# Kernel tuning notes

Measured on AMD Instinct MI355X. Metric: run time of the kernel, lower is better.

The kernel has to match this reference:

```python
import jax, jax.numpy as jnp
import numpy as np

B, H, W, N = 8, 384, 384, 96
STEPSZ = 0.1; ALPHA = 0.01; BETA = 0.01; STD = 1.0
NSTEPS = 50; NSTEPS_W = 10; DMAX = 15.0; EXTGRADFAC = 10.0

def make_gauss_edge_fltr(std):
    # Gaussian-derivative edge filters, one per spatial dim: [2,1,k,k]
    r = int(np.ceil(3 * std)); t = np.arange(-r, r + 1, dtype=np.float32)
    g = np.exp(-t * t / (2 * std * std)); g /= g.sum()
    dg = -t / (std * std) * np.exp(-t * t / (2 * std * std)); dg /= np.abs(dg).sum()
    fy = np.outer(dg, g)   # d/drow
    fx = np.outer(g, dg)   # d/dcol
    return np.stack([fy, fx])[:, None].astype(np.float32)

def setup_inputs() -> dict:
    key = jax.random.key(0)
    k1, k2 = jax.random.split(key, 2)
    pred_dmap = jax.random.normal(k1, (B, 1, H, W), jnp.float32)
    nodes = jax.random.uniform(k2, (B, N, 2), jnp.float32)
    nodes = nodes * jnp.array([H - 1.0, W - 1.0], jnp.float32)
    nodes = jnp.sort(nodes, axis=1)  # roughly monotone chain -> path-like snake
    widths = jnp.ones((B, N), jnp.float32) * 3.0
    fltr = jnp.asarray(make_gauss_edge_fltr(STD))
    return {"pred_dmap": pred_dmap, "nodes": nodes, "widths": widths, "fltr": fltr}

def grad_im(x, fltr):
    # x: [B,1,H,W], fltr: [2,1,k,k] -> [B,2,H,W]
    return jax.lax.conv_general_dilated(x, fltr, (1, 1), 'SAME',
                                        dimension_numbers=('NCHW', 'OIHW', 'NCHW'))

def interp(img, pts):
    # bilinear sample: img [C,H,W], pts [N,2] (row,col) -> [N,C]
    C, Hh, Ww = img.shape
    y = jnp.clip(pts[:, 0], 0.0, Hh - 1.0); x = jnp.clip(pts[:, 1], 0.0, Ww - 1.0)
    y0 = jnp.floor(y).astype(jnp.int32); x0 = jnp.floor(x).astype(jnp.int32)
    y1 = jnp.minimum(y0 + 1, Hh - 1); x1 = jnp.minimum(x0 + 1, Ww - 1)
    wy = y - y0; wx = x - x0
    v00 = img[:, y0, x0]; v01 = img[:, y0, x1]
    v10 = img[:, y1, x0]; v11 = img[:, y1, x1]
    v = v00 * (1 - wy) * (1 - wx) + v01 * (1 - wy) * wx + v10 * wy * (1 - wx) + v11 * wy * wx
    return v.T

def d2_open(x):
    # second difference with replicated endpoints (open snake)
    xp = jnp.concatenate([x[:1], x, x[-1:]], 0)
    return xp[:-2] - 2 * xp[1:-1] + xp[2:]

def snake_one(nodes, widths, g, gw):
    # explicit active-contour iterations on node positions
    def pstep(x, _):
        fext = interp(g, x)                       # [N,2] external force
        d2 = d2_open(x); d4 = d2_open(d2)
        return x + STEPSZ * (ALPHA * d2 - BETA * d4 + fext), None
    x, _ = jax.lax.scan(pstep, nodes, None, length=NSTEPS)
    # unit normals from central-difference tangents
    t = jnp.concatenate([x[1:2] - x[0:1], 0.5 * (x[2:] - x[:-2]), x[-1:] - x[-2:-1]], 0)
    n = jnp.stack([-t[:, 1], t[:, 0]], 1)
    n = n / (jnp.linalg.norm(n, axis=1, keepdims=True) + 1e-6)
    def wstep(w, _):
        gp = interp(gw, x + w[:, None] * n); gm = interp(gw, x - w[:, None] * n)
        f = 0.5 * (jnp.sum(gp * n, 1) - jnp.sum(gm * n, 1))
        return jnp.maximum(w + STEPSZ * f, 0.5), None
    w, _ = jax.lax.scan(wstep, widths, None, length=NSTEPS_W)
    return x, w

def render(x, w):
    # distance-to-ribbon map, clipped at DMAX; only [HW,S] intermediates
    ys, xs = jnp.meshgrid(jnp.arange(H, dtype=jnp.float32),
                          jnp.arange(W, dtype=jnp.float32), indexing='ij')
    P = jnp.stack([ys.ravel(), xs.ravel()], 1)          # [HW,2]
    a = x[:-1]; ab = x[1:] - a                          # [S,2]
    denom = jnp.sum(ab * ab, 1) + 1e-8                  # [S]
    dotpa = P @ ab.T - jnp.sum(a * ab, 1)               # [HW,S] = (P-a).ab
    t = jnp.clip(dotpa / denom, 0.0, 1.0)
    pa2 = jnp.sum(P * P, 1)[:, None] - 2 * (P @ a.T) + jnp.sum(a * a, 1)  # |P-a|^2
    d = jnp.sqrt(jnp.maximum(pa2 - 2 * t * dotpa + t * t * denom, 0.0))
    ws = 0.5 * (w[:-1] + w[1:])                         # per-segment width
    dmap = jnp.min(jnp.maximum(d - ws, 0.0), axis=1)
    return jnp.minimum(dmap, DMAX).reshape(H, W)

def reference(pred_dmap, nodes, widths, fltr):
    gimg = grad_im(pred_dmap, fltr) * EXTGRADFAC          # [B,2,H,W]
    gimgW = grad_im(jnp.abs(pred_dmap), fltr) * EXTGRADFAC
    def per_sample(nd, wd, g, gw):
        x, w = snake_one(nd, wd, g, gw)
        return render(x, w)
    dm = jax.vmap(per_sample)(nodes, widths, gimg, gimgW)[:, None]  # [B,1,H,W]
    dm = jax.lax.stop_gradient(dm)   # snake_dm.detach() in the original
    return jnp.mean((pred_dmap - dm) ** 2)
```

## Files before the change

### kernel.cpp

```cpp
#include <hip/hip_runtime.h>
#include <math.h>

#define BB   8
#define HH   384
#define WW   384
#define NN   96
#define HWSZ (HH * WW)
#define NSEG (NN - 1)
#define SEGF 12
#define SEGPAD 1152
#define DMAXV 15.0f
#define ROWS_PER_BLK 12
#define NCHUNK (HH / ROWS_PER_BLK)
#define CROWS 12
#define CBANDS (HH / CROWS)
#define MAGICU 0x9E3779B9u

typedef unsigned long long u64;
typedef unsigned int u32;

__device__ inline void st_pair(float* p, float lo, float hi)
{
    u64 v = ((u64)__float_as_uint(hi) << 32) | (u64)__float_as_uint(lo);
    __hip_atomic_store((u64*)p, v, __ATOMIC_RELAXED, __HIP_MEMORY_SCOPE_AGENT);
}

__device__ inline float ld_f32_coh(const float* p)
{
    u32 v = __hip_atomic_load((u32*)p, __ATOMIC_RELAXED, __HIP_MEMORY_SCOPE_AGENT);
    return __uint_as_float(v);
}

#define WAIT_ALL() asm volatile("s_waitcnt vmcnt(0) lgkmcnt(0)" ::: "memory")

__device__ inline void load_taps(const float* __restrict__ fltr,
                                 float* __restrict__ sg, float* __restrict__ sdg)
{
    int tid = threadIdx.x;
    if (tid < 7) {
        float s = 0.f;
#pragma unroll
        for (int i = 0; i < 7; ++i) s += fabsf(fltr[i * 7 + tid]);
        sg[tid] = s;
    } else if (tid < 14) {
        int r = tid - 7;
        float s = 0.f;
#pragma unroll
        for (int j = 0; j < 7; ++j) s += fltr[r * 7 + j];
        sdg[r] = s;
    }
    __syncthreads();
}

__device__ inline float2 bilin2i(const float2* __restrict__ img, float py, float px)
{
    float y = fminf(fmaxf(py, 0.0f), (float)(HH - 1));
    float x = fminf(fmaxf(px, 0.0f), (float)(WW - 1));
    int y0 = (int)floorf(y);
    int x0 = (int)floorf(x);
    int y1 = min(y0 + 1, HH - 1);
    bool xedge = (x0 + 1 > WW - 1);
    float wy = y - (float)y0;
    float wx = x - (float)x0;
    float4 r0 = *(const float4*)(img + y0 * WW + x0);
    float4 r1 = *(const float4*)(img + y1 * WW + x0);
    float2 v00 = make_float2(r0.x, r0.y);
    float2 v01 = xedge ? v00 : make_float2(r0.z, r0.w);
    float2 v10 = make_float2(r1.x, r1.y);
    float2 v11 = xedge ? v10 : make_float2(r1.z, r1.w);
    float w00 = (1.f - wy) * (1.f - wx);
    float w01 = (1.f - wy) * wx;
    float w10 = wy * (1.f - wx);
    float w11 = wy * wx;
    return make_float2(v00.x * w00 + v01.x * w01 + v10.x * w10 + v11.x * w11,
                       v00.y * w00 + v01.y * w01 + v10.y * w10 + v11.y * w11);
}

__device__ inline void write_seg_wt(float* __restrict__ r,
                                    float py, float px, float qy, float qx, float wseg)
{
    float aby = qy - py, abx = qx - px;
    float denom = aby * aby + abx * abx + 1e-8f;
    float aab = py * aby + px * abx;
    float aa  = py * py + px * px;
    float reach = DMAXV + wseg;
    st_pair(r + 0,  py,  px);
    st_pair(r + 2,  aby, abx);
    st_pair(r + 4,  aab, denom);
    st_pair(r + 6,  1.0f / denom, aa);
    st_pair(r + 8,  wseg, fminf(py, qy) - reach);
    st_pair(r + 10, fmaxf(py, qy) + reach, 0.f);
}

__global__ __launch_bounds__(384) void snake_fused(
    const float* __restrict__ pred, const float* __restrict__ nodes,
    const float* __restrict__ widths, const float* __restrict__ fltr,
    float* __restrict__ g2f, float* __restrict__ gw2f,
    float* __restrict__ segs, u64* __restrict__ pflag,
    u32* __restrict__ convflag, u32* __restrict__ segflag,
    float* __restrict__ out)
{
    __shared__ float sg[7], sdg[7];
    __shared__ float ss[NSEG * SEGF];
    __shared__ int slo, shi;
    __shared__ float swsum[6];

    int blk = blockIdx.x;
    int b   = blk & 7;
    int band = blk >> 3;
    int t = threadIdx.x;

    load_taps(fltr, sg, sdg);

    {
        int y0 = band * CROWS;
        int x = t;
        const float* pb = pred + (size_t)b * HWSZ;
        bool xin = (x >= 3) && (x < WW - 3);

        float hg[7], hd[7], hga[7], hda[7];

#pragma unroll
        for (int q = 0; q < CROWS + 6; ++q) {
            float vg = 0.f, vd = 0.f, vga = 0.f, vda = 0.f;
            int r = y0 + q - 3;
            if (r >= 0 && r < HH) {
                const float* row = pb + r * WW;
                if (xin) {
#pragma unroll
                    for (int k = 0; k < 7; ++k) {
                        float v  = row[x + k - 3];
                        float av = fabsf(v);
                        vg  = fmaf(v,  sg[k],  vg);
                        vd  = fmaf(v,  sdg[k], vd);
                        vga = fmaf(av, sg[k],  vga);
                        vda = fmaf(av, sdg[k], vda);
                    }
                } else {
#pragma unroll
                    for (int k = 0; k < 7; ++k) {
                        int ix = x + k - 3;
                        float v  = (ix >= 0 && ix < WW) ? row[ix] : 0.f;
                        float av = fabsf(v);
                        vg  = fmaf(v,  sg[k],  vg);
                        vd  = fmaf(v,  sdg[k], vd);
                        vga = fmaf(av, sg[k],  vga);
                        vda = fmaf(av, sdg[k], vda);
                    }
                }
            }
            hg[q % 7] = vg; hd[q % 7] = vd; hga[q % 7] = vga; hda[q % 7] = vda;

            if (q >= 6) {
                int y = y0 + q - 6;
                float o0 = 0.f, o1 = 0.f, o2 = 0.f, o3 = 0.f;
#pragma unroll
                for (int j = 0; j < 7; ++j) {
                    int s = (q - 6 + j) % 7;
                    o0 = fmaf(hg[s],  sdg[j], o0);
                    o1 = fmaf(hd[s],  sg[j],  o1);
                    o2 = fmaf(hga[s], sdg[j], o2);
                    o3 = fmaf(hda[s], sg[j],  o3);
                }
                size_t gi = (size_t)b * HWSZ + (size_t)y * WW + x;
                st_pair(g2f  + 2 * gi, o0 * 10.f, o1 * 10.f);
                st_pair(gw2f + 2 * gi, o2 * 10.f, o3 * 10.f);
            }
        }
    }
    WAIT_ALL();
    __syncthreads();
    if (t == 0)
        __hip_atomic_store(&convflag[blk], MAGICU,
                           __ATOMIC_RELAXED, __HIP_MEMORY_SCOPE_AGENT);

    if (blk < 8 && t < 64) {
        while (__hip_atomic_load(&convflag[b + 8 * (t & 31)],
                                 __ATOMIC_RELAXED, __HIP_MEMORY_SCOPE_AGENT) != MAGICU)
            __builtin_amdgcn_s_sleep(2);
        asm volatile("" ::: "memory");

        const float2* gb  = (const float2*)g2f  + (size_t)b * HWSZ;
        const float2* gwb = (const float2*)gw2f + (size_t)b * HWSZ;
        const int HALF = NN / 2;
        bool act = (t < HALF);
        bool t0 = (t == 0), tl = (t == HALF - 1);

        float ay = 0.f, ax = 0.f, by = 0.f, bx = 0.f;
        if (act) {
            float4 n4 = *(const float4*)(nodes + (size_t)(b * NN + 2 * t) * 2);
            ay = n4.x; ax = n4.y; by = n4.z; bx = n4.w;
        }

        for (int s = 0; s < 50; ++s) {
            float2 fa = bilin2i(gb, ay, ax);
            float2 fb = bilin2i(gb, by, bx);

            float aLy = __shfl_up(ay, 1, 64),  aLx = __shfl_up(ax, 1, 64);
            float bLy = __shfl_up(by, 1, 64),  bLx = __shfl_up(bx, 1, 64);
            float aRy = __shfl_down(ay, 1, 64), aRx = __shfl_down(ax, 1, 64);
            float bRy = __shfl_down(by, 1, 64), bRx = __shfl_down(bx, 1, 64);
            bLy = t0 ? ay : bLy;  bLx = t0 ? ax : bLx;
            aRy = tl ? by : aRy;  aRx = tl ? bx : aRx;

            float d2m_y = aLy - 2.f * bLy + ay;
            float d2a_y = bLy - 2.f * ay + by;
            float d2b_y = ay  - 2.f * by + aRy;
            float d2p_y = by  - 2.f * aRy + bRy;
            d2m_y = t0 ? d2a_y : d2m_y;
            d2p_y = tl ? d2b_y : d2p_y;
            float d4a_y = d2m_y - 2.f * d2a_y + d2b_y;
            float d4b_y = d2a_y - 2.f * d2b_y + d2p_y;

            float d2m_x = aLx - 2.f * bLx + ax;
            float d2a_x = bLx - 2.f * ax + bx;
            float d2b_x = ax  - 2.f * bx + aRx;
            float d2p_x = bx  - 2.f * aRx + bRx;
            d2m_x = t0 ? d2a_x : d2m_x;
            d2p_x = tl ? d2b_x : d2p_x;
            float d4a_x = d2m_x - 2.f * d2a_x + d2b_x;
            float d4b_x = d2a_x - 2.f * d2b_x + d2p_x;

            ay += 0.1f * (0.01f * d2a_y - 0.01f * d4a_y + fa.x);
            ax += 0.1f * (0.01f * d2a_x - 0.01f * d4a_x + fa.y);
            by += 0.1f * (0.01f * d2b_y - 0.01f * d4b_y + fb.x);
            bx += 0.1f * (0.01f * d2b_x - 0.01f * d4b_x + fb.y);
        }

        {
            float bLy = __shfl_up(by, 1, 64), bLx = __shfl_up(bx, 1, 64);
            float aRy = __shfl_down(ay, 1, 64), aRx = __shfl_down(ax, 1, 64);
            float tay = 0.5f * (by - bLy), tax = 0.5f * (bx - bLx);
            if (t0) { tay = by - ay; tax = bx - ax; }
            float tby = 0.5f * (aRy - ay), tbx = 0.5f * (aRx - ax);
            if (tl) { tby = by - ay; tbx = bx - ax; }

            float na0 = -tax, na1 = tay;
            float nrm = sqrtf(na0 * na0 + na1 * na1) + 1e-6f;
            float nay = na0 / nrm, nax = na1 / nrm;
            float nb0 = -tbx, nb1 = tby;
            nrm = sqrtf(nb0 * nb0 + nb1 * nb1) + 1e-6f;
            float nby = nb0 / nrm, nbx = nb1 / nrm;

            float wa = 0.f, wb = 0.f;
            if (act) { wa = widths[b * NN + 2 * t]; wb = widths[b * NN + 2 * t + 1]; }
            for (int s = 0; s < 10; ++s) {
                float2 pa = bilin2i(gwb, ay + wa * nay, ax + wa * nax);
                float2 ma = bilin2i(gwb, ay - wa * nay, ax - wa * nax);
                float2 pb2 = bilin2i(gwb, by + wb * nby, bx + wb * nbx);
                float2 mb = bilin2i(gwb, by - wb * nby, bx - wb * nbx);
                float fa = 0.5f * ((pa.x * nay + pa.y * nax) - (ma.x * nay + ma.y * nax));
                float fb = 0.5f * ((pb2.x * nby + pb2.y * nbx) - (mb.x * nby + mb.y * nbx));
                wa = fmaxf(wa + 0.1f * fa, 0.5f);
                wb = fmaxf(wb + 0.1f * fb, 0.5f);
            }

            float aRy2 = __shfl_down(ay, 1, 64), aRx2 = __shfl_down(ax, 1, 64);
            float waR  = __shfl_down(wa, 1, 64);
            float* segb = segs + (size_t)b * SEGPAD;
            if (act) {
                write_seg_wt(segb + (size_t)(2 * t) * SEGF, ay, ax, by, bx,
                             0.5f * (wa + wb));
                if (t < HALF - 1)
                    write_seg_wt(segb + (size_t)(2 * t + 1) * SEGF, by, bx, aRy2, aRx2,
                                 0.5f * (wb + waR));
            }
        }
        WAIT_ALL();
        if (t == 0)
            __hip_atomic_store(&segflag[b], MAGICU,
                               __ATOMIC_RELAXED, __HIP_MEMORY_SCOPE_AGENT);
    } else if (blk >= 8 && t == 0) {
        while (__hip_atomic_load(&segflag[b],
                                 __ATOMIC_RELAXED, __HIP_MEMORY_SCOPE_AGENT) != MAGICU)
            __builtin_amdgcn_s_sleep(8);
        asm volatile("" ::: "memory");
    }

    if (t == 0) { slo = NSEG; shi = -1; }
    __syncthreads();

    {
        int y0 = band * ROWS_PER_BLK;
        const float* sb = segs + (size_t)b * SEGPAD;
        for (int j = t; j < NSEG * SEGF; j += 384)
            ss[j] = ld_f32_coh(sb + j);
        __syncthreads();

        float cy0 = (float)y0, cy1 = (float)(y0 + ROWS_PER_BLK - 1);
        if (t < NSEG) {
            float ylo = ss[t * SEGF + 9];
            float yhi = ss[t * SEGF + 10];
            if (yhi >= cy0 && ylo <= cy1) {
                atomicMin(&slo, t);
                atomicMax(&shi, t);
            }
        }
        __syncthreads();
        int lo = slo, hi = shi;

        float px = (float)t;
        float px2 = px * px;
        float minv[ROWS_PER_BLK];
#pragma unroll
        for (int r = 0; r < ROWS_PER_BLK; ++r) minv[r] = DMAXV;

        for (int si = lo; si <= hi; ++si) {
            const float* r = ss + si * SEGF;
            float ax = r[1], abx = r[3], ws = r[8];
            float bxe = ax + abx;
            float reach = DMAXV + ws + 0.01f;
            if (px < fminf(ax, bxe) - reach || px > fmaxf(ax, bxe) + reach) continue;

            float ay = r[0], aby = r[2];
            float aab = r[4], denom = r[5], invd = r[6], aa = r[7];
            float dotpa_b = fmaf(px, abx, -aab);
            float pa2_b   = fmaf(px, -2.0f * ax, px2 + aa);
#pragma unroll
            for (int ry = 0; ry < ROWS_PER_BLK; ++ry) {
                float py = (float)(y0 + ry);
                float dotpa = fmaf(py, aby, dotpa_b);
                float tt = fminf(fmaxf(dotpa * invd, 0.0f), 1.0f);
                float pa2 = fmaf(py, fmaf(py, 1.0f, -2.0f * ay), pa2_b);
                float d2 = fmaf(tt, fmaf(tt, denom, -2.0f * dotpa), pa2);
                float d = sqrtf(fmaxf(d2, 0.0f));
                float v = fmaxf(d - ws, 0.0f);
                minv[ry] = fminf(minv[ry], v);
            }
        }

        const float* pb = pred + (size_t)b * HWSZ + (size_t)y0 * WW + t;
        float sq = 0.f;
#pragma unroll
        for (int ry = 0; ry < ROWS_PER_BLK; ++ry) {
            float diff = pb[ry * WW] - minv[ry];
            sq = fmaf(diff, diff, sq);
        }

#pragma unroll
        for (int off = 32; off > 0; off >>= 1) sq += __shfl_down(sq, off, 64);
        if ((t & 63) == 0) swsum[t >> 6] = sq;
        __syncthreads();
        if (t == 0) {
            float tot = swsum[0] + swsum[1] + swsum[2] + swsum[3] + swsum[4] + swsum[5];
            u64 pv = ((u64)MAGICU << 32) | (u64)__float_as_uint(tot);
            __hip_atomic_store(&pflag[blk], pv,
                               __ATOMIC_RELAXED, __HIP_MEMORY_SCOPE_AGENT);
        }
    }

    if (blk == 8) {
        __syncthreads();
        float v = 0.f;
        if (t < 256) {
            u64 pv = __hip_atomic_load(&pflag[t], __ATOMIC_RELAXED,
                                       __HIP_MEMORY_SCOPE_AGENT);
            while ((u32)(pv >> 32) != MAGICU) {
                __builtin_amdgcn_s_sleep(4);
                pv = __hip_atomic_load(&pflag[t], __ATOMIC_RELAXED,
                                       __HIP_MEMORY_SCOPE_AGENT);
            }
            v = __uint_as_float((u32)pv);
        }
#pragma unroll
        for (int off = 32; off > 0; off >>= 1) v += __shfl_down(v, off, 64);
        if ((t & 63) == 0) swsum[t >> 6] = v;
        __syncthreads();
        if (t == 0) {
            float tot = swsum[0] + swsum[1] + swsum[2] + swsum[3] + swsum[4] + swsum[5];
            out[0] = tot * (1.0f / (float)(BB * HWSZ));
        }
    }
}

extern "C" void kernel_launch(void* const* d_in, const int* in_sizes, int n_in,
                              void* d_out, int out_size, void* d_ws, size_t ws_size,
                              hipStream_t stream)
{
    const float* pred   = (const float*)d_in[0];
    const float* nodes  = (const float*)d_in[1];
    const float* widths = (const float*)d_in[2];
    const float* fltr   = (const float*)d_in[3];
    float* out = (float*)d_out;

    float* ws   = (float*)d_ws;
    float* g2   = ws;
    float* gw2  = g2 + (size_t)2 * BB * HWSZ;
    float* segs = gw2 + (size_t)2 * BB * HWSZ;
    float* tail = segs + (size_t)BB * SEGPAD + 256;
    u64* pflag = (u64*)tail;
    u32* convflag = (u32*)(pflag + 256);
    u32* segflag  = convflag + 256;

    snake_fused<<<BB * CBANDS, 384, 0, stream>>>(pred, nodes, widths, fltr,
                                                 g2, gw2, segs, pflag,
                                                 convflag, segflag, out);
}
```

Before: 125.0 us.

## Split convolution into separate kernel, replacing inter-block flag sync with launch boundary

Moves the separable Gaussian-derivative convolution into its own kernel and launches the snake/render kernel after it. The launch boundary replaces the spin-wait on per-band conv flags, and the conv stores become plain vector stores instead of relaxed atomics. The pred rows used by the loss are now prefetched into registers early, so that load overlaps the wait on the segment flag. The cost is an extra kernel launch and losing any overlap between convolution and the snake iterations.

```diff
diff --git a/kernel.cpp b/kernel.cpp
--- a/kernel.cpp
+++ b/kernel.cpp
@@ -50,6 +50,72 @@
         sdg[r] = s;
     }
     __syncthreads();
+}
+
+__global__ __launch_bounds__(384) void conv_fused(
+    const float* __restrict__ pred, const float* __restrict__ fltr,
+    float2* __restrict__ g2, float2* __restrict__ gw2)
+{
+    __shared__ float sg[7], sdg[7];
+    load_taps(fltr, sg, sdg);
+
+    int blk = blockIdx.x;
+    int b = blk & 7;
+    int band = blk >> 3;
+    int y0 = band * CROWS;
+    int x = threadIdx.x;
+    const float* pb = pred + (size_t)b * HWSZ;
+    bool xin = (x >= 3) && (x < WW - 3);
+
+    float hg[7], hd[7], hga[7], hda[7];
+
+#pragma unroll
+    for (int q = 0; q < CROWS + 6; ++q) {
+        float vg = 0.f, vd = 0.f, vga = 0.f, vda = 0.f;
+        int r = y0 + q - 3;
+        if (r >= 0 && r < HH) {
+            const float* row = pb + r * WW;
+            if (xin) {
+#pragma unroll
+                for (int k = 0; k < 7; ++k) {
+                    float v  = row[x + k - 3];
+                    float av = fabsf(v);
+                    vg  = fmaf(v,  sg[k],  vg);
+                    vd  = fmaf(v,  sdg[k], vd);
+                    vga = fmaf(av, sg[k],  vga);
+                    vda = fmaf(av, sdg[k], vda);
+                }
+            } else {
+#pragma unroll
+                for (int k = 0; k < 7; ++k) {
+                    int ix = x + k - 3;
+                    float v  = (ix >= 0 && ix < WW) ? row[ix] : 0.f;
+                    float av = fabsf(v);
+                    vg  = fmaf(v,  sg[k],  vg);
+                    vd  = fmaf(v,  sdg[k], vd);
+                    vga = fmaf(av, sg[k],  vga);
+                    vda = fmaf(av, sdg[k], vda);
+                }
+            }
+        }
+        hg[q % 7] = vg; hd[q % 7] = vd; hga[q % 7] = vga; hda[q % 7] = vda;
+
+        if (q >= 6) {
+            int y = y0 + q - 6;
+            float o0 = 0.f, o1 = 0.f, o2 = 0.f, o3 = 0.f;
+#pragma unroll
+            for (int j = 0; j < 7; ++j) {
+                int s = (q - 6 + j) % 7;
+                o0 = fmaf(hg[s],  sdg[j], o0);
+                o1 = fmaf(hd[s],  sg[j],  o1);
+                o2 = fmaf(hga[s], sdg[j], o2);
+                o3 = fmaf(hda[s], sg[j],  o3);
+            }
+            size_t gi = (size_t)b * HWSZ + (size_t)y * WW + x;
+            g2[gi]  = make_float2(o0 * 10.f, o1 * 10.f);
+            gw2[gi] = make_float2(o2 * 10.f, o3 * 10.f);
+        }
+    }
 }
 
 __device__ inline float2 bilin2i(const float2* __restrict__ img, float py, float px)
@@ -92,15 +158,13 @@
     st_pair(r + 10, fmaxf(py, qy) + reach, 0.f);
 }
 
-__global__ __launch_bounds__(384) void snake_fused(
+__global__ __launch_bounds__(384) void snake_render(
     const float* __restrict__ pred, const float* __restrict__ nodes,
-    const float* __restrict__ widths, const float* __restrict__ fltr,
-    float* __restrict__ g2f, float* __restrict__ gw2f,
+    const float* __restrict__ widths,
+    const float* __restrict__ g2f, const float* __restrict__ gw2f,
     float* __restrict__ segs, u64* __restrict__ pflag,
-    u32* __restrict__ convflag, u32* __restrict__ segflag,
-    float* __restrict__ out)
-{
-    __shared__ float sg[7], sdg[7];
+    u32* __restrict__ segflag, float* __restrict__ out)
+{
     __shared__ float ss[NSEG * SEGF];
     __shared__ int slo, shi;
     __shared__ float swsum[6];
@@ -110,76 +174,15 @@
     int band = blk >> 3;
     int t = threadIdx.x;
 
-    load_taps(fltr, sg, sdg);
-
-    {
-        int y0 = band * CROWS;
-        int x = t;
-        const float* pb = pred + (size_t)b * HWSZ;
-        bool xin = (x >= 3) && (x < WW - 3);
-
-        float hg[7], hd[7], hga[7], hda[7];
-
-#pragma unroll
-        for (int q = 0; q < CROWS + 6; ++q) {
-            float vg = 0.f, vd = 0.f, vga = 0.f, vda = 0.f;
-            int r = y0 + q - 3;
-            if (r >= 0 && r < HH) {
-                const float* row = pb + r * WW;
-                if (xin) {
-#pragma unroll
-                    for (int k = 0; k < 7; ++k) {
-                        float v  = row[x + k - 3];
-                        float av = fabsf(v);
-                        vg  = fmaf(v,  sg[k],  vg);
-                        vd  = fmaf(v,  sdg[k], vd);
-                        vga = fmaf(av, sg[k],  vga);
-                        vda = fmaf(av, sdg[k], vda);
-                    }
-                } else {
-#pragma unroll
-                    for (int k = 0; k < 7; ++k) {
-                        int ix = x + k - 3;
-                        float v  = (ix >= 0 && ix < WW) ? row[ix] : 0.f;
-                        float av = fabsf(v);
-                        vg  = fmaf(v,  sg[k],  vg);
-                        vd  = fmaf(v,  sdg[k], vd);
-                        vga = fmaf(av, sg[k],  vga);
-                        vda = fmaf(av, sdg[k], vda);
-                    }
-                }
-            }
-            hg[q % 7] = vg; hd[q % 7] = vd; hga[q % 7] = vga; hda[q % 7] = vda;
-
-            if (q >= 6) {
-                int y = y0 + q - 6;
-                float o0 = 0.f, o1 = 0.f, o2 = 0.f, o3 = 0.f;
-#pragma unroll
-                for (int j = 0; j < 7; ++j) {
-                    int s = (q - 6 + j) % 7;
-                    o0 = fmaf(hg[s],  sdg[j], o0);
-                    o1 = fmaf(hd[s],  sg[j],  o1);
-                    o2 = fmaf(hga[s], sdg[j], o2);
-                    o3 = fmaf(hda[s], sg[j],  o3);
-                }
-                size_t gi = (size_t)b * HWSZ + (size_t)y * WW + x;
-                st_pair(g2f  + 2 * gi, o0 * 10.f, o1 * 10.f);
-                st_pair(gw2f + 2 * gi, o2 * 10.f, o3 * 10.f);
-            }
-        }
-    }
-    WAIT_ALL();
-    __syncthreads();
-    if (t == 0)
-        __hip_atomic_store(&convflag[blk], MAGICU,
-                           __ATOMIC_RELAXED, __HIP_MEMORY_SCOPE_AGENT);
+    int y0r = band * ROWS_PER_BLK;
+    const float* pb = pred + (size_t)b * HWSZ + (size_t)y0r * WW + t;
+    float pv[ROWS_PER_BLK];
+#pragma unroll
+    for (int ry = 0; ry < ROWS_PER_BLK; ++ry) pv[ry] = pb[ry * WW];
+
+    if (t == 0) { slo = NSEG; shi = -1; }
 
     if (blk < 8 && t < 64) {
-        while (__hip_atomic_load(&convflag[b + 8 * (t & 31)],
-                                 __ATOMIC_RELAXED, __HIP_MEMORY_SCOPE_AGENT) != MAGICU)
-            __builtin_amdgcn_s_sleep(2);
-        asm volatile("" ::: "memory");
-
         const float2* gb  = (const float2*)g2f  + (size_t)b * HWSZ;
         const float2* gwb = (const float2*)gw2f + (size_t)b * HWSZ;
         const int HALF = NN / 2;
@@ -277,11 +280,10 @@
         asm volatile("" ::: "memory");
     }
 
-    if (t == 0) { slo = NSEG; shi = -1; }
     __syncthreads();
 
     {
-        int y0 = band * ROWS_PER_BLK;
+        int y0 = y0r;
         const float* sb = segs + (size_t)b * SEGPAD;
         for (int j = t; j < NSEG * SEGF; j += 384)
             ss[j] = ld_f32_coh(sb + j);
@@ -329,11 +331,10 @@
             }
         }
 
-        const float* pb = pred + (size_t)b * HWSZ + (size_t)y0 * WW + t;
         float sq = 0.f;
 #pragma unroll
         for (int ry = 0; ry < ROWS_PER_BLK; ++ry) {
-            float diff = pb[ry * WW] - minv[ry];
+            float diff = pv[ry] - minv[ry];
             sq = fmaf(diff, diff, sq);
         }
 
@@ -343,8 +344,8 @@
         __syncthreads();
         if (t == 0) {
             float tot = swsum[0] + swsum[1] + swsum[2] + swsum[3] + swsum[4] + swsum[5];
-            u64 pv = ((u64)MAGICU << 32) | (u64)__float_as_uint(tot);
-            __hip_atomic_store(&pflag[blk], pv,
+            u64 pvv = ((u64)MAGICU << 32) | (u64)__float_as_uint(tot);
+            __hip_atomic_store(&pflag[blk], pvv,
                                __ATOMIC_RELAXED, __HIP_MEMORY_SCOPE_AGENT);
         }
     }
@@ -353,14 +354,14 @@
         __syncthreads();
         float v = 0.f;
         if (t < 256) {
-            u64 pv = __hip_atomic_load(&pflag[t], __ATOMIC_RELAXED,
-                                       __HIP_MEMORY_SCOPE_AGENT);
-            while ((u32)(pv >> 32) != MAGICU) {
+            u64 pvv = __hip_atomic_load(&pflag[t], __ATOMIC_RELAXED,
+                                        __HIP_MEMORY_SCOPE_AGENT);
+            while ((u32)(pvv >> 32) != MAGICU) {
                 __builtin_amdgcn_s_sleep(4);
-                pv = __hip_atomic_load(&pflag[t], __ATOMIC_RELAXED,
-                                       __HIP_MEMORY_SCOPE_AGENT);
-            }
-            v = __uint_as_float((u32)pv);
+                pvv = __hip_atomic_load(&pflag[t], __ATOMIC_RELAXED,
+                                        __HIP_MEMORY_SCOPE_AGENT);
+            }
+            v = __uint_as_float((u32)pvv);
         }
 #pragma unroll
         for (int off = 32; off > 0; off >>= 1) v += __shfl_down(v, off, 64);
@@ -389,10 +390,10 @@
     float* segs = gw2 + (size_t)2 * BB * HWSZ;
     float* tail = segs + (size_t)BB * SEGPAD + 256;
     u64* pflag = (u64*)tail;
-    u32* convflag = (u32*)(pflag + 256);
-    u32* segflag  = convflag + 256;
-
-    snake_fused<<<BB * CBANDS, 384, 0, stream>>>(pred, nodes, widths, fltr,
-                                                 g2, gw2, segs, pflag,
-                                                 convflag, segflag, out);
-}
+    u32* segflag = (u32*)(pflag + 256);
+
+    conv_fused<<<BB * CBANDS, 384, 0, stream>>>(pred, fltr,
+                                                (float2*)g2, (float2*)gw2);
+    snake_render<<<BB * NCHUNK, 384, 0, stream>>>(pred, nodes, widths, g2, gw2,
+                                                  segs, pflag, segflag, out);
+}
```

Result: no change. 127.1 us (+1.7%).
